# Performance work log

Measured on AMD Instinct MI355X. Metric: run time of the kernel, lower is better.

The kernel has to match this reference:

```python
import jax, jax.numpy as jnp
import numpy as np

B, IN, OUT, M = 4096, 512, 512, 16


def setup_inputs() -> dict:
    key = jax.random.key(0)
    k1, k2, k3 = jax.random.split(key, 3)
    # inputs kept strictly positive and inside the physical range [0, 60]
    x = jax.random.uniform(k1, (B, IN), jnp.float32, 0.1, 10.0)
    # photonic basis coefficients: positive, with small polynomial terms
    b_coef = jax.random.uniform(k2, (M, 8), jnp.float32, 0.1, 0.9)
    b_coef = b_coef.at[:, 4:].multiply(0.01)
    coeffs = 0.01 * jax.random.normal(k3, (OUT, IN, M), jnp.float32)
    return {"x": x, "coeffs": coeffs, "b_coef": b_coef}


def _photonic_basis(x, b):
    # x: (B, IN) -> broadcast against M basis functions -> (B, IN, M)
    xe = x[:, :, None]                                   # (B, IN, 1)
    b1, b2, b3, b4, b5, b6, b7, b8 = [b[:, i][None, None, :] for i in range(8)]
    inner = jnp.expm1(b3 * xe)
    powered = jnp.power(inner, b4)
    y = (b1 * jnp.log(1.0 + b2 * jnp.log1p(powered))
         + b5 * xe + b6 * xe**2 + b7 * xe**3 + b8 * xe**4)
    return y


def reference(x, coeffs, b_coef):
    # basis: (B, IN, M); double reduce over (IN, M) == GEMM of size B x (IN*M) x OUT
    basis = _photonic_basis(x, b_coef)
    y = jnp.einsum('bim,oim->bo', basis, coeffs)         # (B, OUT)
    return y
```

## Files before the change

### kernel.cpp

```cpp
#include <hip/hip_runtime.h>
#include <hip/hip_bf16.h>
#include <stdint.h>

#define B_DIM   4096
#define IN_DIM  512
#define OUT_DIM 512
#define M_DIM   16
#define K_DIM   (IN_DIM * M_DIM)
#define MN      (B_DIM * OUT_DIM)

typedef unsigned short ushort_t;
typedef __attribute__((ext_vector_type(8))) __bf16 bf16x8;
typedef __attribute__((ext_vector_type(2))) __bf16 bf16x2;
typedef __attribute__((ext_vector_type(4))) float  f32x4;

__device__ __forceinline__ ushort_t f2bf(float f) {
  union { float f; uint32_t u; } v; v.f = f;
  uint32_t u = v.u + 0x7fffu + ((v.u >> 16) & 1u);
  return (ushort_t)(u >> 16);
}

__device__ __forceinline__ uint32_t pkbf(float lo, float hi) {
  union { bf16x2 h; uint32_t u; } v;
  v.h[0] = (__bf16)lo; v.h[1] = (__bf16)hi;
  return v.u;
}

__device__ __forceinline__ float rfl(float f) {
  union { float f; int i; } v; v.f = f;
  v.i = __builtin_amdgcn_readfirstlane(v.i);
  return v.f;
}

#define CONV_N4 (OUT_DIM * K_DIM / 4)
__global__ __launch_bounds__(256) void convert_coeffs_kernel(
    const float* __restrict__ src, ushort_t* __restrict__ dst) {
  int i = blockIdx.x * 256 + threadIdx.x;
  float4 v = ((const float4*)src)[i];
  ushort4 o;
  o.x = f2bf(v.x); o.y = f2bf(v.y); o.z = f2bf(v.z); o.w = f2bf(v.w);
  ((ushort4*)dst)[i] = o;
}

#define BM 128
#define BN 512
#define BK 32
#define SPLITK 8
#define KC (K_DIM / SPLITK)
#define NITER (KC / BK)
#define XCOLS (KC / M_DIM)
#define XPAD  129

#define GLD16(g, l) \
  __builtin_amdgcn_global_load_lds((const __attribute__((address_space(1))) void*)(g), \
                                   (__attribute__((address_space(3))) void*)(l), 16, 0, 0)

#define WAIT_BAR(N) \
  asm volatile("s_waitcnt vmcnt(" #N ") lgkmcnt(0)\n\ts_barrier" ::: "memory")

template <int ATOMIC>
__global__ __launch_bounds__(512, 2) void gemm_kernel(
    const float* __restrict__ x,
    const ushort_t* __restrict__ Bt,
    const float* __restrict__ bc,
    float* __restrict__ P) {
  __shared__ __align__(16) ushort_t As[2][BM * BK];
  __shared__ __align__(16) ushort_t Bs[3][BN * BK];
  __shared__ __align__(16) float    Xs[XCOLS * XPAD];
  const int tid  = threadIdx.x;
  const int wave = tid >> 6;
  const int lane = tid & 63;
  const int wgid = blockIdx.x;
  const int ks = wgid & 7, bm = wgid >> 3;

  {
    const int r = tid >> 2, q = tid & 3;
    const float4* xrow = (const float4*)(x + (size_t)(bm * BM + r) * IN_DIM + ks * XCOLS);
    #pragma unroll
    for (int j = 0; j < 4; ++j) {
      float4 v = xrow[q * 4 + j];
      Xs[(q * 16 + j * 4 + 0) * XPAD + r] = v.x;
      Xs[(q * 16 + j * 4 + 1) * XPAD + r] = v.y;
      Xs[(q * 16 + j * 4 + 2) * XPAD + r] = v.z;
      Xs[(q * 16 + j * 4 + 3) * XPAD + r] = v.w;
    }
  }

  const int srow = wave * 16 + (lane >> 2);
  const int scol = (((lane & 3) ^ ((lane >> 3) & 3)) * 8);
  const ushort_t* Bg0 = Bt + (size_t)srow * K_DIM + ks * KC + scol;
  const ushort_t* Bg1 = Bg0 + (size_t)128 * K_DIM;
  const ushort_t* Bg2 = Bg0 + (size_t)256 * K_DIM;
  const ushort_t* Bg3 = Bg0 + (size_t)384 * K_DIM;
  const int bofs0 = (wave * 16) * BK;
  const int bofs1 = (128 + wave * 16) * BK;
  const int bofs2 = (256 + wave * 16) * BK;
  const int bofs3 = (384 + wave * 16) * BK;

#define STAGEB(lb) do { \
    GLD16(Bg0, &Bs[lb][bofs0]); GLD16(Bg1, &Bs[lb][bofs1]); \
    GLD16(Bg2, &Bs[lb][bofs2]); GLD16(Bg3, &Bs[lb][bofs3]); \
    Bg0 += BK; Bg1 += BK; Bg2 += BK; Bg3 += BK; } while (0)

  const int half = wave & 1;
  const int arow = (wave >> 1) * 32 + (lane >> 1);
  const int il   = lane & 1;
  const int aslot = ((il * 2 + half) ^ ((lane >> 2) & 3));
  const int awe   = arow * BK + aslot * 8;
  const int xbase = il * XPAD + arow;

  const float LOG2E = 1.44269504088896340736f;
  const float LN2   = 0.69314718055994530942f;
  float c1[8], c2[8], c3[8], c4[8], c5[8], c6[8], c7[8], c8[8];
  {
    const float* bch = bc + half * 64;
    #pragma unroll
    for (int m = 0; m < 8; ++m) {
      c1[m] = rfl(rfl(bch[m*8+0]) * LN2); c2[m] = rfl(rfl(bch[m*8+1]) * LN2);
      c3[m] = rfl(bch[m*8+2]); c4[m] = rfl(bch[m*8+3]);
      c5[m] = rfl(bch[m*8+4]); c6[m] = rfl(bch[m*8+5]);
      c7[m] = rfl(bch[m*8+6]); c8[m] = rfl(bch[m*8+7]);
    }
  }

#define BASIS(ab, t) do { \
    float xv = Xs[xbase + 2 * XPAD * (t)]; \
    float xl2 = xv * LOG2E; \
    float x2 = xv * xv, x3 = x2 * xv, x4 = x2 * x2; \
    float ym[8]; \
    _Pragma("unroll") \
    for (int mi = 0; mi < 8; ++mi) { \
      float e     = __builtin_amdgcn_exp2f(c3[mi] * xl2); \
      float inner = e - 1.0f; \
      float p     = __builtin_amdgcn_exp2f(c4[mi] * __builtin_amdgcn_logf(inner)); \
      float L1    = __builtin_amdgcn_logf(1.0f + p); \
      float vv    = __builtin_amdgcn_logf(1.0f + c2[mi] * L1); \
      ym[mi] = c1[mi] * vv + c5[mi] * xv + c6[mi] * x2 + c7[mi] * x3 + c8[mi] * x4; \
    } \
    *(uint4*)(&As[ab][awe]) = make_uint4(pkbf(ym[0], ym[1]), pkbf(ym[2], ym[3]), \
                                         pkbf(ym[4], ym[5]), pkbf(ym[6], ym[7])); \
  } while (0)

  const int wr = wave >> 2, wc = wave & 3;
  const int fm = lane & 15;
  const int fkswz = (((lane >> 4) ^ ((lane >> 1) & 3)) << 3);

  f32x4 acc[4][8] = {};

#define COMPUTE(ab, lb) do { \
    bf16x8 af[4], bfv[8]; \
    _Pragma("unroll") \
    for (int t2 = 0; t2 < 4; ++t2) \
      af[t2] = *(const bf16x8*)&As[ab][(wr * 64 + t2 * 16 + fm) * BK + fkswz]; \
    _Pragma("unroll") \
    for (int u = 0; u < 8; ++u) \
      bfv[u] = *(const bf16x8*)&Bs[lb][(wc * 128 + u * 16 + fm) * BK + fkswz]; \
    __builtin_amdgcn_s_setprio(1); \
    _Pragma("unroll") \
    for (int mt = 0; mt < 4; ++mt) \
      _Pragma("unroll") \
      for (int nt = 0; nt < 8; ++nt) \
        acc[mt][nt] = __builtin_amdgcn_mfma_f32_16x16x32_bf16(af[mt], bfv[nt], acc[mt][nt], 0, 0, 0); \
    __builtin_amdgcn_s_setprio(0); \
  } while (0)

#define STEP(lbN, ap, ac, lb, t1) do { \
    STAGEB(lbN); BASIS(ap, t1); COMPUTE(ac, lb); WAIT_BAR(4); } while (0)

  STAGEB(0); STAGEB(1);
  __syncthreads();
  BASIS(0, 0);
  WAIT_BAR(0);

  for (int tb = 0; tb < NITER - 2; tb += 6) {
    STEP(2, 1, 0, 0, tb + 1);
    STEP(0, 0, 1, 1, tb + 2);
    STEP(1, 1, 0, 2, tb + 3);
    STEP(2, 0, 1, 0, tb + 4);
    STEP(0, 1, 0, 1, tb + 5);
    STEP(1, 0, 1, 2, tb + 6);
  }
  BASIS(1, NITER - 1);
  COMPUTE(0, 0);
  WAIT_BAR(0);
  COMPUTE(1, 1);

  if (ATOMIC) {
    const int colb = wc * 128 + fm;
    const int rowb = bm * BM + wr * 64 + (lane >> 4) * 4;
    #pragma unroll
    for (int mt = 0; mt < 4; ++mt)
      #pragma unroll
      for (int nt = 0; nt < 8; ++nt)
        #pragma unroll
        for (int j = 0; j < 4; ++j)
          atomicAdd(P + (size_t)(rowb + mt * 16 + j) * OUT_DIM + (colb + nt * 16),
                    acc[mt][nt][j]);
  } else {
    float* dst = P + (size_t)ks * MN + (size_t)bm * (BM * BN)
                   + wave * 8192 + lane * 4;
    #pragma unroll
    for (int mt = 0; mt < 4; ++mt)
      #pragma unroll
      for (int nt = 0; nt < 8; ++nt)
        *(f32x4*)(dst + (mt * 8 + nt) * 256) = acc[mt][nt];
  }
#undef STAGEB
#undef BASIS
#undef COMPUTE
#undef STEP
}

__global__ __launch_bounds__(256) void reduce_kernel(
    const float* __restrict__ P, float* __restrict__ out) {
  int i = blockIdx.x * 256 + threadIdx.x;
  const float4* p = (const float4*)P;
  float4 r = p[i];
  #pragma unroll
  for (int s = 1; s < SPLITK; ++s) {
    float4 v = p[i + (size_t)s * (MN / 4)];
    r.x += v.x; r.y += v.y; r.z += v.z; r.w += v.w;
  }
  int bm   = i >> 14;
  int rem  = i & 16383;
  int wv   = rem >> 11;
  int rem2 = rem & 2047;
  int mtnt = rem2 >> 6;
  int lane = rem2 & 63;
  int mt = mtnt >> 3, nt = mtnt & 7;
  int wr = wv >> 2,  wc = wv & 3;
  int row = bm * BM + wr * 64 + mt * 16 + (lane >> 4) * 4;
  int col = wc * 128 + nt * 16 + (lane & 15);
  float* o = out + (size_t)row * OUT_DIM + col;
  o[0 * OUT_DIM] = r.x;
  o[1 * OUT_DIM] = r.y;
  o[2 * OUT_DIM] = r.z;
  o[3 * OUT_DIM] = r.w;
}

extern "C" void kernel_launch(void* const* d_in, const int* in_sizes, int n_in,
                              void* d_out, int out_size, void* d_ws, size_t ws_size,
                              hipStream_t stream) {
  const float* x      = (const float*)d_in[0];
  const float* coeffs = (const float*)d_in[1];
  const float* b_coef = (const float*)d_in[2];
  float* out = (float*)d_out;
  char*  ws  = (char*)d_ws;

  const size_t COEF_BYTES = (size_t)OUT_DIM * K_DIM * 2;
  ushort_t* coefb = (ushort_t*)ws;
  float* partials = (float*)(ws + COEF_BYTES);
  const size_t FULL = COEF_BYTES + (size_t)SPLITK * MN * 4;
  const bool use_atomic = (ws_size < FULL);

  convert_coeffs_kernel<<<CONV_N4 / 256, 256, 0, stream>>>(coeffs, coefb);

  const int nblk = (B_DIM / BM) * SPLITK;
  if (use_atomic) {
    hipMemsetAsync(d_out, 0, (size_t)MN * 4, stream);
    gemm_kernel<1><<<nblk, 512, 0, stream>>>(x, coefb, b_coef, out);
  } else {
    gemm_kernel<0><<<nblk, 512, 0, stream>>>(x, coefb, b_coef, partials);
    reduce_kernel<<<MN / 4 / 256, 256, 0, stream>>>(partials, out);
  }
}
```

Before: 137.0 us.

## Restructure GEMM main loop into fine-grained barrier phases interleaving MFMA, loads, basis

```diff
diff --git a/kernel.cpp b/kernel.cpp
--- a/kernel.cpp
+++ b/kernel.cpp
@@ -55,8 +55,11 @@
   __builtin_amdgcn_global_load_lds((const __attribute__((address_space(1))) void*)(g), \
                                    (__attribute__((address_space(3))) void*)(l), 16, 0, 0)
 
-#define WAIT_BAR(N) \
-  asm volatile("s_waitcnt vmcnt(" #N ") lgkmcnt(0)\n\ts_barrier" ::: "memory")
+#define BARX()   asm volatile("s_barrier" ::: "memory")
+#define LGKM0()  asm volatile("s_waitcnt lgkmcnt(0)" ::: "memory")
+#define EPI_L()  asm volatile("s_waitcnt lgkmcnt(0)\n\ts_barrier" ::: "memory")
+#define EPI_V4() asm volatile("s_waitcnt vmcnt(4) lgkmcnt(0)\n\ts_barrier" ::: "memory")
+#define EPI_V0() asm volatile("s_waitcnt vmcnt(0) lgkmcnt(0)\n\ts_barrier" ::: "memory")
 
 template <int ATOMIC>
 __global__ __launch_bounds__(512, 2) void gemm_kernel(
@@ -64,7 +67,7 @@
     const ushort_t* __restrict__ Bt,
     const float* __restrict__ bc,
     float* __restrict__ P) {
-  __shared__ __align__(16) ushort_t As[2][BM * BK];
+  __shared__ __align__(16) ushort_t As[3][BM * BK];
   __shared__ __align__(16) ushort_t Bs[3][BN * BK];
   __shared__ __align__(16) float    Xs[XCOLS * XPAD];
   const int tid  = threadIdx.x;
@@ -97,11 +100,6 @@
   const int bofs2 = (256 + wave * 16) * BK;
   const int bofs3 = (384 + wave * 16) * BK;
 
-#define STAGEB(lb) do { \
-    GLD16(Bg0, &Bs[lb][bofs0]); GLD16(Bg1, &Bs[lb][bofs1]); \
-    GLD16(Bg2, &Bs[lb][bofs2]); GLD16(Bg3, &Bs[lb][bofs3]); \
-    Bg0 += BK; Bg1 += BK; Bg2 += BK; Bg3 += BK; } while (0)
-
   const int half = wave & 1;
   const int arow = (wave >> 1) * 32 + (lane >> 1);
   const int il   = lane & 1;
@@ -123,22 +121,21 @@
     }
   }
 
-#define BASIS(ab, t) do { \
-    float xv = Xs[xbase + 2 * XPAD * (t)]; \
+#define BASIS4(ab, t_, mi0) do { \
+    float xv = Xs[xbase + 2 * XPAD * (t_)]; \
     float xl2 = xv * LOG2E; \
     float x2 = xv * xv, x3 = x2 * xv, x4 = x2 * x2; \
-    float ym[8]; \
+    float ym[4]; \
     _Pragma("unroll") \
-    for (int mi = 0; mi < 8; ++mi) { \
-      float e     = __builtin_amdgcn_exp2f(c3[mi] * xl2); \
+    for (int mi = 0; mi < 4; ++mi) { int mm = (mi0) + mi; \
+      float e     = __builtin_amdgcn_exp2f(c3[mm] * xl2); \
       float inner = e - 1.0f; \
-      float p     = __builtin_amdgcn_exp2f(c4[mi] * __builtin_amdgcn_logf(inner)); \
+      float p     = __builtin_amdgcn_exp2f(c4[mm] * __builtin_amdgcn_logf(inner)); \
       float L1    = __builtin_amdgcn_logf(1.0f + p); \
-      float vv    = __builtin_amdgcn_logf(1.0f + c2[mi] * L1); \
-      ym[mi] = c1[mi] * vv + c5[mi] * xv + c6[mi] * x2 + c7[mi] * x3 + c8[mi] * x4; \
+      float vv    = __builtin_amdgcn_logf(1.0f + c2[mm] * L1); \
+      ym[mi] = c1[mm] * vv + c5[mm] * xv + c6[mm] * x2 + c7[mm] * x3 + c8[mm] * x4; \
     } \
-    *(uint4*)(&As[ab][awe]) = make_uint4(pkbf(ym[0], ym[1]), pkbf(ym[2], ym[3]), \
-                                         pkbf(ym[4], ym[5]), pkbf(ym[6], ym[7])); \
+    *(uint2*)(&As[ab][awe + (mi0)]) = make_uint2(pkbf(ym[0], ym[1]), pkbf(ym[2], ym[3])); \
   } while (0)
 
   const int wr = wave >> 2, wc = wave & 3;
@@ -147,43 +144,69 @@
 
   f32x4 acc[4][8] = {};
 
-#define COMPUTE(ab, lb) do { \
-    bf16x8 af[4], bfv[8]; \
+#define LD_AF(s) do { _Pragma("unroll") \
+    for (int t2 = 0; t2 < 4; ++t2) \
+      af[t2] = *(const bf16x8*)&As[s][(wr * 64 + t2 * 16 + fm) * BK + fkswz]; } while (0)
+#define LD_B2(s, q) do { \
+    b0 = *(const bf16x8*)&Bs[s][(wc * 128 + (2*(q))    * 16 + fm) * BK + fkswz]; \
+    b1 = *(const bf16x8*)&Bs[s][(wc * 128 + (2*(q)+1)  * 16 + fm) * BK + fkswz]; } while (0)
+#define MF8(q) do { __builtin_amdgcn_s_setprio(1); \
     _Pragma("unroll") \
-    for (int t2 = 0; t2 < 4; ++t2) \
-      af[t2] = *(const bf16x8*)&As[ab][(wr * 64 + t2 * 16 + fm) * BK + fkswz]; \
-    _Pragma("unroll") \
-    for (int u = 0; u < 8; ++u) \
-      bfv[u] = *(const bf16x8*)&Bs[lb][(wc * 128 + u * 16 + fm) * BK + fkswz]; \
-    __builtin_amdgcn_s_setprio(1); \
-    _Pragma("unroll") \
-    for (int mt = 0; mt < 4; ++mt) \
-      _Pragma("unroll") \
-      for (int nt = 0; nt < 8; ++nt) \
-        acc[mt][nt] = __builtin_amdgcn_mfma_f32_16x16x32_bf16(af[mt], bfv[nt], acc[mt][nt], 0, 0, 0); \
-    __builtin_amdgcn_s_setprio(0); \
+    for (int mt = 0; mt < 4; ++mt) { \
+      acc[mt][2*(q)]   = __builtin_amdgcn_mfma_f32_16x16x32_bf16(af[mt], b0, acc[mt][2*(q)],   0, 0, 0); \
+      acc[mt][2*(q)+1] = __builtin_amdgcn_mfma_f32_16x16x32_bf16(af[mt], b1, acc[mt][2*(q)+1], 0, 0, 0); \
+    } __builtin_amdgcn_s_setprio(0); } while (0)
+
+#define ITER(sA, sB, sP, sQ, tp_) do { \
+    bf16x8 af[4], b0, b1; \
+     LD_AF(sA); LD_B2(sA, 0); GLD16(Bg0, &Bs[sP][bofs0]); \
+    BARX(); LGKM0(); MF8(0); EPI_L(); \
+     LD_B2(sA, 1); GLD16(Bg1, &Bs[sP][bofs1]); \
+    BARX(); LGKM0(); MF8(1); BASIS4(sP, (tp_), 0); EPI_L(); \
+     LD_B2(sA, 2); GLD16(Bg2, &Bs[sP][bofs2]); \
+    BARX(); LGKM0(); MF8(2); BASIS4(sP, (tp_), 4); EPI_L(); \
+     LD_B2(sA, 3); GLD16(Bg3, &Bs[sP][bofs3]); \
+    Bg0 += BK; Bg1 += BK; Bg2 += BK; Bg3 += BK; \
+    BARX(); LGKM0(); MF8(3); EPI_V4(); \
+     LD_AF(sB); LD_B2(sB, 0); GLD16(Bg0, &Bs[sQ][bofs0]); \
+    BARX(); LGKM0(); MF8(0); EPI_L(); \
+     LD_B2(sB, 1); GLD16(Bg1, &Bs[sQ][bofs1]); \
+    BARX(); LGKM0(); MF8(1); BASIS4(sQ, (tp_) + 1, 0); EPI_L(); \
+     LD_B2(sB, 2); GLD16(Bg2, &Bs[sQ][bofs2]); \
+    BARX(); LGKM0(); MF8(2); BASIS4(sQ, (tp_) + 1, 4); EPI_L(); \
+     LD_B2(sB, 3); GLD16(Bg3, &Bs[sQ][bofs3]); \
+    Bg0 += BK; Bg1 += BK; Bg2 += BK; Bg3 += BK; \
+    BARX(); LGKM0(); MF8(3); EPI_V4(); \
   } while (0)
 
-#define STEP(lbN, ap, ac, lb, t1) do { \
-    STAGEB(lbN); BASIS(ap, t1); COMPUTE(ac, lb); WAIT_BAR(4); } while (0)
-
-  STAGEB(0); STAGEB(1);
+  GLD16(Bg0, &Bs[0][bofs0]); GLD16(Bg1, &Bs[0][bofs1]);
+  GLD16(Bg2, &Bs[0][bofs2]); GLD16(Bg3, &Bs[0][bofs3]);
+  Bg0 += BK; Bg1 += BK; Bg2 += BK; Bg3 += BK;
+  GLD16(Bg0, &Bs[1][bofs0]); GLD16(Bg1, &Bs[1][bofs1]);
+  GLD16(Bg2, &Bs[1][bofs2]); GLD16(Bg3, &Bs[1][bofs3]);
+  Bg0 += BK; Bg1 += BK; Bg2 += BK; Bg3 += BK;
   __syncthreads();
-  BASIS(0, 0);
-  WAIT_BAR(0);
-
-  for (int tb = 0; tb < NITER - 2; tb += 6) {
-    STEP(2, 1, 0, 0, tb + 1);
-    STEP(0, 0, 1, 1, tb + 2);
-    STEP(1, 1, 0, 2, tb + 3);
-    STEP(2, 0, 1, 0, tb + 4);
-    STEP(0, 1, 0, 1, tb + 5);
-    STEP(1, 0, 1, 2, tb + 6);
-  }
-  BASIS(1, NITER - 1);
-  COMPUTE(0, 0);
-  WAIT_BAR(0);
-  COMPUTE(1, 1);
+  BASIS4(0, 0, 0); BASIS4(0, 0, 4);
+  BASIS4(1, 1, 0); BASIS4(1, 1, 4);
+  EPI_L();
+
+  for (int ii = 0, tp = 2; ii < 5; ++ii, tp += 6) {
+    ITER(0, 1, 2, 0, tp);
+    ITER(2, 0, 1, 2, tp + 2);
+    ITER(1, 2, 0, 1, tp + 4);
+  }
+
+  {
+    bf16x8 af[4], b0, b1;
+    LD_AF(0); LD_B2(0, 0); BARX(); LGKM0(); MF8(0); EPI_L();
+    LD_B2(0, 1);           BARX(); LGKM0(); MF8(1); EPI_L();
+    LD_B2(0, 2);           BARX(); LGKM0(); MF8(2); EPI_L();
+    LD_B2(0, 3);           BARX(); LGKM0(); MF8(3); EPI_V0();
+    LD_AF(1); LD_B2(1, 0); BARX(); LGKM0(); MF8(0); EPI_L();
+    LD_B2(1, 1);           BARX(); LGKM0(); MF8(1); EPI_L();
+    LD_B2(1, 2);           BARX(); LGKM0(); MF8(2); EPI_L();
+    LD_B2(1, 3);           BARX(); LGKM0(); MF8(3);
+  }
 
   if (ATOMIC) {
     const int colb = wc * 128 + fm;
@@ -205,10 +228,11 @@
       for (int nt = 0; nt < 8; ++nt)
         *(f32x4*)(dst + (mt * 8 + nt) * 256) = acc[mt][nt];
   }
-#undef STAGEB
-#undef BASIS
-#undef COMPUTE
-#undef STEP
+#undef BASIS4
+#undef LD_AF
+#undef LD_B2
+#undef MF8
+#undef ITER
 }
 
 __global__ __launch_bounds__(256) void reduce_kernel(
```

New measurement: 148.2 us. 8.2% more time.
